# Kernel optimization log

Hardware: AMD Instinct MI355X
Metric: run time of the kernel (lower is better)

## Reference

```python
import jax, jax.numpy as jnp
import numpy as np
from jax import lax

BETA = 10.0
TAU = 0.25
V_MIN = 0.0
V_MAX = 1.0
NUM_THRESHOLDS = 4


def _inverse_sigmoid(x):
    eps = 1e-06
    x = np.clip(x, eps, 1 - eps)
    return np.log(x / (1 - x))


def setup_inputs() -> dict:
    key = jax.random.key(0)
    k1, _ = jax.random.split(key)
    T, B, C, H, W = 16, 32, 128, 32, 32
    x = jax.random.normal(k1, (T, B, C, H, W), dtype=jnp.float32)
    # parameter init as in the torch module: inverse_sigmoid of linspace(0.1, 0.9)
    values = np.linspace(0.1, 0.9, NUM_THRESHOLDS)
    init_raw = _inverse_sigmoid((values - V_MIN) / (V_MAX - V_MIN))
    v_thresholds_raw = jnp.asarray(init_raw, dtype=jnp.float32)
    return {"x": x, "v_thresholds_raw": v_thresholds_raw}


def reference(x, v_thresholds_raw):
    # thresholds in (v_min, v_max): [K]
    thresholds = V_MIN + (V_MAX - V_MIN) * jax.nn.sigmoid(v_thresholds_raw)

    def step(carry, x_t):
        mem, prev_spike = carry
        # LIF membrane update with soft reset by previous spike count
        u = TAU * mem * (1.0 - prev_spike) + x_t            # [B,C,H,W]
        # soft spike count: sum of sigmoids over thresholds
        s = jax.nn.sigmoid(BETA * (u[..., None] - thresholds)).sum(-1)  # [B,C,H,W]
        return (u, s), s

    zero = jnp.zeros_like(x[0])
    _, out = lax.scan(step, (zero, zero), x)  # out: [T,B,C,H,W]
    return out
```

## Files before the change

kernel.cpp:

```cpp
#include <hip/hip_runtime.h>


#define T_STEPS 16
#define NTHR 4

__device__ __forceinline__ float fast_sigmoid(float z) {
    return __builtin_amdgcn_rcpf(1.0f + __expf(-z));
}

__global__ __launch_bounds__(256) void lif_spike_kernel(
    const float* __restrict__ x,
    const float* __restrict__ raw_thr,
    float* __restrict__ out,
    int n4 ) {

    int i = blockIdx.x * blockDim.x + threadIdx.x;
    if (i >= n4) return;

    float thr[NTHR];
#pragma unroll
    for (int k = 0; k < NTHR; ++k) {
        thr[k] = fast_sigmoid(raw_thr[k]);
    }

    const float4* __restrict__ xv = reinterpret_cast<const float4*>(x);
    float4* __restrict__ ov = reinterpret_cast<float4*>(out);

    float mem0 = 0.f, mem1 = 0.f, mem2 = 0.f, mem3 = 0.f;
    float spk0 = 0.f, spk1 = 0.f, spk2 = 0.f, spk3 = 0.f;

    const float BETA = 10.0f;
    const float TAU = 0.25f;

#pragma unroll
    for (int t = 0; t < T_STEPS; ++t) {
        float4 xt = xv[(size_t)t * (size_t)n4 + (size_t)i];

        float u0 = TAU * mem0 * (1.0f - spk0) + xt.x;
        float u1 = TAU * mem1 * (1.0f - spk1) + xt.y;
        float u2 = TAU * mem2 * (1.0f - spk2) + xt.z;
        float u3 = TAU * mem3 * (1.0f - spk3) + xt.w;

        float s0 = 0.f, s1 = 0.f, s2 = 0.f, s3 = 0.f;
#pragma unroll
        for (int k = 0; k < NTHR; ++k) {
            s0 += fast_sigmoid(BETA * (u0 - thr[k]));
            s1 += fast_sigmoid(BETA * (u1 - thr[k]));
            s2 += fast_sigmoid(BETA * (u2 - thr[k]));
            s3 += fast_sigmoid(BETA * (u3 - thr[k]));
        }

        mem0 = u0; mem1 = u1; mem2 = u2; mem3 = u3;
        spk0 = s0; spk1 = s1; spk2 = s2; spk3 = s3;

        float4 o; o.x = s0; o.y = s1; o.z = s2; o.w = s3;
        ov[(size_t)t * (size_t)n4 + (size_t)i] = o;
    }
}

extern "C" void kernel_launch(void* const* d_in, const int* in_sizes, int n_in,
                              void* d_out, int out_size, void* d_ws, size_t ws_size,
                              hipStream_t stream) {
    const float* x = (const float*)d_in[0];
    const float* raw_thr = (const float*)d_in[1];
    float* out = (float*)d_out;

    int n_spatial = in_sizes[0] / T_STEPS;
    int n4 = n_spatial / 4;

    const int block = 256;
    const int grid = (n4 + block - 1) / block;

    lif_spike_kernel<<<grid, block, 0, stream>>>(x, raw_thr, out, n4);
}
```

Before: 110.0 us.

## Factor sigmoid exponentials, preload all timesteps, use nontemporal loads and stores

The sigmoid sum is rewritten algebraically as 1/(1+E*c_k), with E=exp2(-S*u) computed once per element and c_k=exp2(S*thr_k) precomputed. This cuts the exp count from four per element per timestep to one. All 16 timesteps are loaded up front with nontemporal loads to raise memory-level parallelism, and outputs use nontemporal stores. Register pressure rises from holding 64 floats of input, and the factored form can overflow for extreme u, where E*c_k becomes inf and the rcp result goes to zero.

```diff
diff --git a/kernel.cpp b/kernel.cpp
--- a/kernel.cpp
+++ b/kernel.cpp
@@ -4,9 +4,7 @@
 #define T_STEPS 16
 #define NTHR 4
 
-__device__ __forceinline__ float fast_sigmoid(float z) {
-    return __builtin_amdgcn_rcpf(1.0f + __expf(-z));
-}
+typedef float v4f __attribute__((ext_vector_type(4)));
 
 __global__ __launch_bounds__(256) void lif_spike_kernel(
     const float* __restrict__ x,
@@ -17,59 +15,63 @@
     int i = blockIdx.x * blockDim.x + threadIdx.x;
     if (i >= n4) return;
 
-    float thr[NTHR];
+    constexpr float LOG2E = 1.44269504088896340736f;
+    constexpr float BETA  = 10.0f;
+    constexpr float TAU   = 0.25f;
+    constexpr float S     = BETA * LOG2E;
+
+    float ck[NTHR];
 #pragma unroll
     for (int k = 0; k < NTHR; ++k) {
-        thr[k] = fast_sigmoid(raw_thr[k]);
+        float r   = raw_thr[k];
+        float thr = __builtin_amdgcn_rcpf(1.0f + __builtin_amdgcn_exp2f(-LOG2E * r));
+        ck[k] = __builtin_amdgcn_exp2f(S * thr);
     }
 
-    const float4* __restrict__ xv = reinterpret_cast<const float4*>(x);
-    float4* __restrict__ ov = reinterpret_cast<float4*>(out);
+    const v4f* xv = reinterpret_cast<const v4f*>(x) + i;
+    v4f*       ov = reinterpret_cast<v4f*>(out) + i;
 
-    float mem0 = 0.f, mem1 = 0.f, mem2 = 0.f, mem3 = 0.f;
-    float spk0 = 0.f, spk1 = 0.f, spk2 = 0.f, spk3 = 0.f;
+    v4f xt[T_STEPS];
+#pragma unroll
+    for (int t = 0; t < T_STEPS; ++t)
+        xt[t] = __builtin_nontemporal_load(xv + (size_t)t * (size_t)n4);
 
-    const float BETA = 10.0f;
-    const float TAU = 0.25f;
+    float mem[4] = {0.f, 0.f, 0.f, 0.f};
+    float spk[4] = {0.f, 0.f, 0.f, 0.f};
 
 #pragma unroll
     for (int t = 0; t < T_STEPS; ++t) {
-        float4 xt = xv[(size_t)t * (size_t)n4 + (size_t)i];
-
-        float u0 = TAU * mem0 * (1.0f - spk0) + xt.x;
-        float u1 = TAU * mem1 * (1.0f - spk1) + xt.y;
-        float u2 = TAU * mem2 * (1.0f - spk2) + xt.z;
-        float u3 = TAU * mem3 * (1.0f - spk3) + xt.w;
-
-        float s0 = 0.f, s1 = 0.f, s2 = 0.f, s3 = 0.f;
+        float s[4];
 #pragma unroll
-        for (int k = 0; k < NTHR; ++k) {
-            s0 += fast_sigmoid(BETA * (u0 - thr[k]));
-            s1 += fast_sigmoid(BETA * (u1 - thr[k]));
-            s2 += fast_sigmoid(BETA * (u2 - thr[k]));
-            s3 += fast_sigmoid(BETA * (u3 - thr[k]));
+        for (int j = 0; j < 4; ++j) {
+            float tm = TAU * mem[j];
+            float u  = __builtin_fmaf(-tm, spk[j], tm) + xt[t][j];
+            float E  = __builtin_amdgcn_exp2f(-S * u);
+            float acc = 0.f;
+#pragma unroll
+            for (int k = 0; k < NTHR; ++k)
+                acc += __builtin_amdgcn_rcpf(__builtin_fmaf(E, ck[k], 1.0f));
+            s[j]   = acc;
+            mem[j] = u;
+            spk[j] = acc;
         }
-
-        mem0 = u0; mem1 = u1; mem2 = u2; mem3 = u3;
-        spk0 = s0; spk1 = s1; spk2 = s2; spk3 = s3;
-
-        float4 o; o.x = s0; o.y = s1; o.z = s2; o.w = s3;
-        ov[(size_t)t * (size_t)n4 + (size_t)i] = o;
+        v4f o = {s[0], s[1], s[2], s[3]};
+        __builtin_nontemporal_store(o, ov + (size_t)t * (size_t)n4);
     }
 }
 
 extern "C" void kernel_launch(void* const* d_in, const int* in_sizes, int n_in,
                               void* d_out, int out_size, void* d_ws, size_t ws_size,
                               hipStream_t stream) {
-    const float* x = (const float*)d_in[0];
+    const float* x       = (const float*)d_in[0];
     const float* raw_thr = (const float*)d_in[1];
-    float* out = (float*)d_out;
+    float*       out     = (float*)d_out;
 
     int n_spatial = in_sizes[0] / T_STEPS;
-    int n4 = n_spatial / 4;
+    int n4        = n_spatial / 4;
 
     const int block = 256;
-    const int grid = (n4 + block - 1) / block;
+    const int grid  = (n4 + block - 1) / block;
 
     lif_spike_kernel<<<grid, block, 0, stream>>>(x, raw_thr, out, n4);
 }
```

New measurement: 118.4 us. +7.6%, slower.
